# Optimization experiments

Hardware: AMD Instinct MI355X
Metric: run time of the kernel (lower is better)

The kernel has to match this reference:

```python
import jax, jax.numpy as jnp
import numpy as np

B, S, D, H = 8, 1024, 1024, 16
DH = D // H


def setup_inputs() -> dict:
    key = jax.random.key(0)
    ks = jax.random.split(key, 7)
    scale = 1.0 / np.sqrt(DH)
    return {
        "sequences": jax.random.normal(ks[0], (B, S, D), dtype=jnp.float32),
        "Wq": jax.random.uniform(ks[1], (H, DH, DH), jnp.float32, -scale, scale),
        "bq": jax.random.uniform(ks[2], (H, DH), jnp.float32, -scale, scale),
        "Wk": jax.random.uniform(ks[3], (H, DH, DH), jnp.float32, -scale, scale),
        "bk": jax.random.uniform(ks[4], (H, DH), jnp.float32, -scale, scale),
        "Wv": jax.random.uniform(ks[5], (H, DH, DH), jnp.float32, -scale, scale),
        "bv": jax.random.uniform(ks[6], (H, DH), jnp.float32, -scale, scale),
    }


def reference(sequences, Wq, bq, Wk, bk, Wv, bv):
    # split channels into heads: [B,S,H,DH]
    x = sequences.reshape(B, S, H, DH)
    # per-head linear maps (torch Linear: y = x @ W.T + b)
    q = jnp.einsum("bshd,hed->bshe", x, Wq) + bq  # [B,S,H,DH]
    k = jnp.einsum("bshd,hed->bshe", x, Wk) + bk
    v = jnp.einsum("bshd,hed->bshe", x, Wv) + bv
    scores = jnp.einsum("bshd,bthd->bhst", q, k) / jnp.sqrt(jnp.asarray(DH, x.dtype))
    attn = jax.nn.softmax(scores, axis=-1)  # [B,H,S,S]
    out = jnp.einsum("bhst,bthd->bshd", attn, v)  # [B,S,H,DH]
    return out.reshape(B, S, D)
```

## Files before the change

### kernel.cpp

```cpp
#include <hip/hip_runtime.h>
#include <hip/hip_bf16.h>


constexpr int NB = 8, NS = 1024, ND = 1024, NH = 16, NDH = 64;

typedef __bf16 bf16x8 __attribute__((ext_vector_type(8)));
typedef __bf16 bf16x2 __attribute__((ext_vector_type(2)));
typedef float f32x4 __attribute__((ext_vector_type(4)));

__device__ __forceinline__ f32x4 mfma16(bf16x8 a, bf16x8 b, f32x4 c) {
  return __builtin_amdgcn_mfma_f32_16x16x32_bf16(a, b, c, 0, 0, 0);
}

__device__ __forceinline__ float fast_exp2(float x) {
#if __has_builtin(__builtin_amdgcn_exp2f)
  return __builtin_amdgcn_exp2f(x);
#else
  return __builtin_exp2f(x);
#endif
}

__device__ __forceinline__ unsigned pack2(float lo, float hi) {
#if __has_builtin(__builtin_amdgcn_cvt_pk_bf16_f32)
  bf16x2 v = __builtin_amdgcn_cvt_pk_bf16_f32(lo, hi);
  return __builtin_bit_cast(unsigned, v);
#else
  unsigned uh = __builtin_bit_cast(unsigned, hi) + 0x8000u;
  unsigned ul = __builtin_bit_cast(unsigned, lo) + 0x8000u;
  return __builtin_amdgcn_perm(uh, ul, 0x07060302u);
#endif
}

__device__ __forceinline__ bf16x8 cvt2bf8(float4 lo, float4 hi) {
  bf16x8 r;
  r[0] = (__bf16)lo.x; r[1] = (__bf16)lo.y; r[2] = (__bf16)lo.z; r[3] = (__bf16)lo.w;
  r[4] = (__bf16)hi.x; r[5] = (__bf16)hi.y; r[6] = (__bf16)hi.z; r[7] = (__bf16)hi.w;
  return r;
}

__device__ __forceinline__ void gload16(const __hip_bfloat16* g, __hip_bfloat16* l) {
  __builtin_amdgcn_global_load_lds(
      (const __attribute__((address_space(1))) void*)g,
      (__attribute__((address_space(3))) void*)l, 16, 0, 0);
}

__global__ __launch_bounds__(256) void qkv_proj_kernel(
    const float* __restrict__ x,
    const float* __restrict__ Wq, const float* __restrict__ bq,
    const float* __restrict__ Wk, const float* __restrict__ bk,
    const float* __restrict__ Wv, const float* __restrict__ bv,
    __hip_bfloat16* __restrict__ Qo, __hip_bfloat16* __restrict__ Ko,
    __hip_bfloat16* __restrict__ Vt) {
  __shared__ __align__(16) __hip_bfloat16 Wlds[3][NDH][72];
  const int tid = threadIdx.x;
  const int wave = tid >> 6, lane = tid & 63;
  const int m = lane & 15, quad = lane >> 4;
  const int h = blockIdx.x & (NH - 1);
  const int sblk = blockIdx.x >> 4;

  const float* Ws[3] = {Wq + h * 4096, Wk + h * 4096, Wv + h * 4096};
#pragma unroll
  for (int mt = 0; mt < 3; mt++) {
#pragma unroll
    for (int p = 0; p < 4; p++) {
      int idx = (p * 256 + tid) * 4;
      float4 v = *(const float4*)(Ws[mt] + idx);
      uint2 w;
      w.x = pack2(v.x, v.y);
      w.y = pack2(v.z, v.w);
      *(uint2*)&Wlds[mt][idx >> 6][idx & 63] = w;
    }
  }
  __syncthreads();

  float bq4[4][4], bk4[4][4], bvv[4];
#pragma unroll
  for (int nt = 0; nt < 4; nt++) {
    float4 a = *(const float4*)(bq + h * 64 + nt * 16 + quad * 4);
    float4 c = *(const float4*)(bk + h * 64 + nt * 16 + quad * 4);
    bq4[nt][0] = a.x; bq4[nt][1] = a.y; bq4[nt][2] = a.z; bq4[nt][3] = a.w;
    bk4[nt][0] = c.x; bk4[nt][1] = c.y; bk4[nt][2] = c.z; bk4[nt][3] = c.w;
    bvv[nt] = bv[h * 64 + nt * 16 + m];
  }

  const int rowbase = sblk * 256 + wave * 64;
  bf16x8 Xf[4][2];
#pragma unroll
  for (int st = 0; st < 4; st++) {
    const float* xp = x + (size_t)(rowbase + st * 16 + m) * ND + h * NDH + quad * 8;
#pragma unroll
    for (int c = 0; c < 2; c++) {
      float4 lo = *(const float4*)(xp + c * 32);
      float4 hi = *(const float4*)(xp + c * 32 + 4);
      Xf[st][c] = cvt2bf8(lo, hi);
    }
  }

  const int b = rowbase >> 10;
  const int s0 = rowbase & 1023;
  const float qscale = 0.18033688011112042f;

#pragma unroll
  for (int mt = 0; mt < 3; mt++) {
#pragma unroll
    for (int nt = 0; nt < 4; nt++) {
      bf16x8 w0 = *(const bf16x8*)&Wlds[mt][nt * 16 + m][quad * 8];
      bf16x8 w1 = *(const bf16x8*)&Wlds[mt][nt * 16 + m][32 + quad * 8];
#pragma unroll
      for (int st = 0; st < 4; st++) {
        f32x4 acc = {0.f, 0.f, 0.f, 0.f};
        if (mt < 2) {
          acc = mfma16(w0, Xf[st][0], acc);
          acc = mfma16(w1, Xf[st][1], acc);
          const int srow = s0 + st * 16 + m;
          uint2 w;
          if (mt == 0) {
            w.x = pack2((acc[0] + bq4[nt][0]) * qscale, (acc[1] + bq4[nt][1]) * qscale);
            w.y = pack2((acc[2] + bq4[nt][2]) * qscale, (acc[3] + bq4[nt][3]) * qscale);
            *(uint2*)(Qo + ((size_t)(b * NH + h) * NS + srow) * NDH +
                      nt * 16 + quad * 4) = w;
          } else {
            w.x = pack2(acc[0] + bk4[nt][0], acc[1] + bk4[nt][1]);
            w.y = pack2(acc[2] + bk4[nt][2], acc[3] + bk4[nt][3]);
            *(uint2*)(Ko + ((size_t)(b * NH + h) * NS + srow) * NDH +
                      nt * 16 + quad * 4) = w;
          }
        } else {
          acc = mfma16(Xf[st][0], w0, acc);
          acc = mfma16(Xf[st][1], w1, acc);
          uint2 w;
          w.x = pack2(acc[0] + bvv[nt], acc[1] + bvv[nt]);
          w.y = pack2(acc[2] + bvv[nt], acc[3] + bvv[nt]);
          *(uint2*)(Vt + ((size_t)(b * NH + h) * NDH + nt * 16 + m) * NS + s0 +
                    st * 16 + quad * 4) = w;
        }
      }
    }
  }
}

__global__ __launch_bounds__(256, 2) void attn_kernel(
    const __hip_bfloat16* __restrict__ Q,
    const __hip_bfloat16* __restrict__ K,
    const __hip_bfloat16* __restrict__ Vt,
    float* __restrict__ out) {
  __shared__ __align__(16) __hip_bfloat16 Kt[2][64][64];
  __shared__ __align__(16) __hip_bfloat16 Vl[2][64][64];

  const int tid = threadIdx.x;
  const int wave = tid >> 6, lane = tid & 63;
  const int m = lane & 15, quad = lane >> 4;

  const int xcd = blockIdx.x & 7;
  const int j = blockIdx.x >> 3;
  const int bh = xcd * 16 + (j & 15);
  const int qblk = j >> 4;
  const int qbase = qblk * 256 + wave * 64;

  const __hip_bfloat16* Qp = Q + (size_t)bh * NS * NDH;
  const __hip_bfloat16* Kp = K + (size_t)bh * NS * NDH;
  const __hip_bfloat16* Vp = Vt + (size_t)bh * NDH * NS;

  bf16x8 Bq[4][2];
#pragma unroll
  for (int g = 0; g < 4; g++)
#pragma unroll
    for (int dh = 0; dh < 2; dh++)
      Bq[g][dh] = *(const bf16x8*)(Qp + (size_t)(qbase + g * 16 + m) * NDH +
                                   dh * 32 + quad * 8);

  f32x4 accO[4][4];
  f32x4 lsum[4];
#pragma unroll
  for (int g = 0; g < 4; g++) {
    lsum[g] = (f32x4){0.f, 0.f, 0.f, 0.f};
#pragma unroll
    for (int nt = 0; nt < 4; nt++) accO[g][nt] = (f32x4){0.f, 0.f, 0.f, 0.f};
  }
  bf16x8 ones8;
#pragma unroll
  for (int i = 0; i < 8; i++) ones8[i] = (__bf16)1.0f;

  const int r8 = lane >> 3;
  const int csV = (lane & 7) ^ r8;
  const int csK0 = (lane & 7) ^ (r8 & 3);
  const int krow = 8 * (m >> 2) + (m & 3);
  const int fK = (m & 3) ^ (((m >> 2) & 1) << 2);
  const int kc0 = (quad ^ fK) * 8;
  const int vc0 = (quad ^ (m & 7)) * 8;

#define STAGE(buf, tb)                                                        \
  {                                                                           \
    _Pragma("unroll") for (int p8 = 0; p8 < 2; p8++) {                        \
      const int row0 = wave * 16 + p8 * 8;                                    \
      gload16(Kp + (size_t)((tb) * 64 + row0 + r8) * NDH +                    \
                  (csK0 ^ (p8 * 4)) * 8,                                      \
              &Kt[buf][row0][0]);                                             \
      gload16(Vp + (size_t)(row0 + r8) * NS + (tb) * 64 + csV * 8,            \
              &Vl[buf][row0][0]);                                             \
    }                                                                         \
  }

  STAGE(0, 0);

  for (int tb = 0; tb < NS / 64; tb++) {
    const int cur = tb & 1;
    __syncthreads();
    if (tb + 1 < NS / 64) STAGE(cur ^ 1, tb + 1);

    bf16x8 Pa[4][2];
#pragma unroll
    for (int c = 0; c < 2; c++) {
      uint2 pw[4][2];
#pragma unroll
      for (int p = 0; p < 2; p++) {
        const __hip_bfloat16* kr = &Kt[cur][c * 32 + 4 * p + krow][0];
        bf16x8 k0 = *(const bf16x8*)(kr + kc0);
        bf16x8 k1 = *(const bf16x8*)(kr + (kc0 ^ 32));
#pragma unroll
        for (int g = 0; g < 4; g++) {
          f32x4 a = {0.f, 0.f, 0.f, 0.f};
          a = mfma16(k0, Bq[g][0], a);
          a = mfma16(k1, Bq[g][1], a);
          pw[g][p].x = pack2(fast_exp2(a[0]), fast_exp2(a[1]));
          pw[g][p].y = pack2(fast_exp2(a[2]), fast_exp2(a[3]));
        }
      }
#pragma unroll
      for (int g = 0; g < 4; g++) {
        uint4 u = {pw[g][0].x, pw[g][0].y, pw[g][1].x, pw[g][1].y};
        Pa[g][c] = __builtin_bit_cast(bf16x8, u);
      }
    }
#pragma unroll
    for (int g = 0; g < 4; g++)
#pragma unroll
      for (int c = 0; c < 2; c++) lsum[g] = mfma16(Pa[g][c], ones8, lsum[g]);
#pragma unroll
    for (int nt = 0; nt < 4; nt++) {
      const __hip_bfloat16* vr = &Vl[cur][nt * 16 + m][0];
      bf16x8 v0 = *(const bf16x8*)(vr + vc0);
      bf16x8 v1 = *(const bf16x8*)(vr + (vc0 ^ 32));
#pragma unroll
      for (int g = 0; g < 4; g++) {
        accO[g][nt] = mfma16(Pa[g][0], v0, accO[g][nt]);
        accO[g][nt] = mfma16(Pa[g][1], v1, accO[g][nt]);
      }
    }
  }
#undef STAGE

  const int b = bh >> 4, h = bh & (NH - 1);
#pragma unroll
  for (int g = 0; g < 4; g++) {
#pragma unroll
    for (int r = 0; r < 4; r++) {
      float inv = 1.0f / lsum[g][r];
      int srow = qbase + g * 16 + quad * 4 + r;
      float* op = out + (size_t)(b * NS + srow) * ND + h * NDH;
#pragma unroll
      for (int nt = 0; nt < 4; nt++) op[nt * 16 + m] = accO[g][nt][r] * inv;
    }
  }
}

extern "C" void kernel_launch(void* const* d_in, const int* in_sizes, int n_in,
                              void* d_out, int out_size, void* d_ws, size_t ws_size,
                              hipStream_t stream) {
  const float* x  = (const float*)d_in[0];
  const float* Wq = (const float*)d_in[1];
  const float* bq = (const float*)d_in[2];
  const float* Wk = (const float*)d_in[3];
  const float* bk = (const float*)d_in[4];
  const float* Wv = (const float*)d_in[5];
  const float* bv = (const float*)d_in[6];
  float* out = (float*)d_out;

  const size_t elems = (size_t)NB * NH * NS * NDH;
  __hip_bfloat16* Qw = (__hip_bfloat16*)d_ws;
  __hip_bfloat16* Kw = Qw + elems;
  __hip_bfloat16* Vw = Kw + elems;

  qkv_proj_kernel<<<512, 256, 0, stream>>>(x, Wq, bq, Wk, bk, Wv, bv, Qw, Kw, Vw);
  attn_kernel<<<512, 256, 0, stream>>>(Qw, Kw, Vw, out);
}
```

Before: 142.2 us.

## Double K/V tile width to 128 keys and use truncating bf16 pack

Each pipeline stage now stages 128 keys of K and V instead of 64, which halves the number of loop iterations and __syncthreads barriers. The K and V swizzles are reworked to fit the wider tiles. The exp-to-bf16 conversion for P now truncates instead of rounding, which removes an add per pack. In exchange the kernel uses twice the LDS (64KB per block), which may limit occupancy to two blocks per CU, and the truncation adds a small bias to P.

Result: no change. 140.3 us (-1.4%).

```diff
diff --git a/kernel.cpp b/kernel.cpp
--- a/kernel.cpp
+++ b/kernel.cpp
@@ -5,7 +5,6 @@
 constexpr int NB = 8, NS = 1024, ND = 1024, NH = 16, NDH = 64;
 
 typedef __bf16 bf16x8 __attribute__((ext_vector_type(8)));
-typedef __bf16 bf16x2 __attribute__((ext_vector_type(2)));
 typedef float f32x4 __attribute__((ext_vector_type(4)));
 
 __device__ __forceinline__ f32x4 mfma16(bf16x8 a, bf16x8 b, f32x4 c) {
@@ -21,14 +20,14 @@
 }
 
 __device__ __forceinline__ unsigned pack2(float lo, float hi) {
-#if __has_builtin(__builtin_amdgcn_cvt_pk_bf16_f32)
-  bf16x2 v = __builtin_amdgcn_cvt_pk_bf16_f32(lo, hi);
-  return __builtin_bit_cast(unsigned, v);
-#else
   unsigned uh = __builtin_bit_cast(unsigned, hi) + 0x8000u;
   unsigned ul = __builtin_bit_cast(unsigned, lo) + 0x8000u;
   return __builtin_amdgcn_perm(uh, ul, 0x07060302u);
-#endif
+}
+
+__device__ __forceinline__ unsigned pack2t(float lo, float hi) {
+  return __builtin_amdgcn_perm(__builtin_bit_cast(unsigned, hi),
+                               __builtin_bit_cast(unsigned, lo), 0x07060302u);
 }
 
 __device__ __forceinline__ bf16x8 cvt2bf8(float4 lo, float4 hi) {
@@ -144,8 +143,8 @@
     const __hip_bfloat16* __restrict__ K,
     const __hip_bfloat16* __restrict__ Vt,
     float* __restrict__ out) {
-  __shared__ __align__(16) __hip_bfloat16 Kt[2][64][64];
-  __shared__ __align__(16) __hip_bfloat16 Vl[2][64][64];
+  __shared__ __align__(16) __hip_bfloat16 Kt[2][128][64];
+  __shared__ __align__(16) __hip_bfloat16 Vl[2][64][128];
 
   const int tid = threadIdx.x;
   const int wave = tid >> 6, lane = tid & 63;
@@ -180,71 +179,74 @@
   bf16x8 ones8;
 #pragma unroll
   for (int i = 0; i < 8; i++) ones8[i] = (__bf16)1.0f;
-
-  const int r8 = lane >> 3;
-  const int csV = (lane & 7) ^ r8;
-  const int csK0 = (lane & 7) ^ (r8 & 3);
+  const f32x4 fzero = {0.f, 0.f, 0.f, 0.f};
+
   const int krow = 8 * (m >> 2) + (m & 3);
   const int fK = (m & 3) ^ (((m >> 2) & 1) << 2);
   const int kc0 = (quad ^ fK) * 8;
-  const int vc0 = (quad ^ (m & 7)) * 8;
+  const int vq = quad ^ (m & 3);
+  const int vm2 = (m >> 2) & 3;
 
 #define STAGE(buf, tb)                                                        \
   {                                                                           \
-    _Pragma("unroll") for (int p8 = 0; p8 < 2; p8++) {                        \
-      const int row0 = wave * 16 + p8 * 8;                                    \
-      gload16(Kp + (size_t)((tb) * 64 + row0 + r8) * NDH +                    \
-                  (csK0 ^ (p8 * 4)) * 8,                                      \
-              &Kt[buf][row0][0]);                                             \
-      gload16(Vp + (size_t)(row0 + r8) * NS + (tb) * 64 + csV * 8,            \
-              &Vl[buf][row0][0]);                                             \
+    _Pragma("unroll") for (int l = 0; l < 4; l++) {                           \
+      const int krb = wave * 32 + l * 8;                                      \
+      const int csK = (lane & 7) ^ ((lane >> 3) & 3) ^ ((l & 1) << 2);        \
+      gload16(Kp + (size_t)((tb) * 128 + krb + (lane >> 3)) * NDH + csK * 8,  \
+              &Kt[buf][krb][0]);                                              \
+      const int vrb = wave * 16 + l * 4;                                      \
+      const int csVl = (lane & 15) ^ (l * 4 + (lane >> 4));                   \
+      gload16(Vp + (size_t)(vrb + (lane >> 4)) * NS + (tb) * 128 + csVl * 8,  \
+              &Vl[buf][vrb][0]);                                              \
     }                                                                         \
   }
 
   STAGE(0, 0);
 
-  for (int tb = 0; tb < NS / 64; tb++) {
+  for (int tb = 0; tb < 8; tb++) {
     const int cur = tb & 1;
     __syncthreads();
-    if (tb + 1 < NS / 64) STAGE(cur ^ 1, tb + 1);
-
-    bf16x8 Pa[4][2];
-#pragma unroll
-    for (int c = 0; c < 2; c++) {
-      uint2 pw[4][2];
-#pragma unroll
-      for (int p = 0; p < 2; p++) {
-        const __hip_bfloat16* kr = &Kt[cur][c * 32 + 4 * p + krow][0];
-        bf16x8 k0 = *(const bf16x8*)(kr + kc0);
-        bf16x8 k1 = *(const bf16x8*)(kr + (kc0 ^ 32));
-#pragma unroll
-        for (int g = 0; g < 4; g++) {
-          f32x4 a = {0.f, 0.f, 0.f, 0.f};
-          a = mfma16(k0, Bq[g][0], a);
-          a = mfma16(k1, Bq[g][1], a);
-          pw[g][p].x = pack2(fast_exp2(a[0]), fast_exp2(a[1]));
-          pw[g][p].y = pack2(fast_exp2(a[2]), fast_exp2(a[3]));
+    if (tb + 1 < 8) STAGE(cur ^ 1, tb + 1);
+
+#pragma unroll
+    for (int h64 = 0; h64 < 2; h64++) {
+      bf16x8 Pa[4][2];
+#pragma unroll
+      for (int c = 0; c < 2; c++) {
+        uint4 u[4];
+#pragma unroll
+        for (int p = 0; p < 2; p++) {
+          const __hip_bfloat16* kr =
+              &Kt[cur][h64 * 64 + c * 32 + 4 * p + krow][0];
+          bf16x8 k0 = *(const bf16x8*)(kr + kc0);
+          bf16x8 k1 = *(const bf16x8*)(kr + (kc0 ^ 32));
+#pragma unroll
+          for (int g = 0; g < 4; g++) {
+            f32x4 a = mfma16(k1, Bq[g][1], mfma16(k0, Bq[g][0], fzero));
+            unsigned w0 = pack2t(fast_exp2(a[0]), fast_exp2(a[1]));
+            unsigned w1 = pack2t(fast_exp2(a[2]), fast_exp2(a[3]));
+            if (p == 0) { u[g].x = w0; u[g].y = w1; }
+            else        { u[g].z = w0; u[g].w = w1; }
+          }
         }
+#pragma unroll
+        for (int g = 0; g < 4; g++) Pa[g][c] = __builtin_bit_cast(bf16x8, u[g]);
       }
 #pragma unroll
-      for (int g = 0; g < 4; g++) {
-        uint4 u = {pw[g][0].x, pw[g][0].y, pw[g][1].x, pw[g][1].y};
-        Pa[g][c] = __builtin_bit_cast(bf16x8, u);
-      }
-    }
-#pragma unroll
-    for (int g = 0; g < 4; g++)
-#pragma unroll
-      for (int c = 0; c < 2; c++) lsum[g] = mfma16(Pa[g][c], ones8, lsum[g]);
-#pragma unroll
-    for (int nt = 0; nt < 4; nt++) {
-      const __hip_bfloat16* vr = &Vl[cur][nt * 16 + m][0];
-      bf16x8 v0 = *(const bf16x8*)(vr + vc0);
-      bf16x8 v1 = *(const bf16x8*)(vr + (vc0 ^ 32));
-#pragma unroll
-      for (int g = 0; g < 4; g++) {
-        accO[g][nt] = mfma16(Pa[g][0], v0, accO[g][nt]);
-        accO[g][nt] = mfma16(Pa[g][1], v1, accO[g][nt]);
+      for (int g = 0; g < 4; g++)
+#pragma unroll
+        for (int c = 0; c < 2; c++) lsum[g] = mfma16(Pa[g][c], ones8, lsum[g]);
+#pragma unroll
+      for (int nt = 0; nt < 4; nt++) {
+#pragma unroll
+        for (int c = 0; c < 2; c++) {
+          const int tb4 = h64 * 2 + c;
+          const int off = (((tb4 ^ vm2) << 2) | vq) << 3;
+          bf16x8 v = *(const bf16x8*)&Vl[cur][nt * 16 + m][off];
+#pragma unroll
+          for (int g = 0; g < 4; g++)
+            accO[g][nt] = mfma16(Pa[g][c], v, accO[g][nt]);
+        }
       }
     }
   }
```
